# Optimization experiments

Measured on AMD Instinct MI355X. Metric: run time of the kernel, lower is better.

## Reference

```python
import jax, jax.numpy as jnp
import numpy as np

EPS = 1e-5
GROUPS = 32


def conv2d(x, w, b):
    # x: [N,C,H,W], w: [O,I,3,3] (or 1x1), stride 1, padding 'same' for 3x3
    kh = w.shape[2]
    pad = (kh - 1) // 2
    y = jax.lax.conv_general_dilated(x, w, (1, 1), ((pad, pad), (pad, pad)),
                                     dimension_numbers=('NCHW', 'OIHW', 'NCHW'))
    return y + b[None, :, None, None]


def group_norm(x, g, b):
    N, C, H, W = x.shape
    xr = x.reshape(N, GROUPS, C // GROUPS, H, W)
    mu = xr.mean(axis=(2, 3, 4), keepdims=True)
    var = xr.var(axis=(2, 3, 4), keepdims=True)
    xr = (xr - mu) / jnp.sqrt(var + EPS)
    return xr.reshape(N, C, H, W) * g[None, :, None, None] + b[None, :, None, None]


def batch_norm(x, g, b):
    # training-mode BatchNorm2d: batch statistics over (N,H,W)
    mu = x.mean(axis=(0, 2, 3), keepdims=True)
    var = x.var(axis=(0, 2, 3), keepdims=True)
    return (x - mu) / jnp.sqrt(var + EPS) * g[None, :, None, None] + b[None, :, None, None]


def binary_activation(x):
    # STE: forward sign(x), backward through piecewise poly out3
    out_fwd = jnp.sign(x)
    m1 = (x < -1).astype(x.dtype)
    m2 = (x < 0).astype(x.dtype)
    m3 = (x < 1).astype(x.dtype)
    out1 = -1.0 * m1 + (x * x + 2.0 * x) * (1.0 - m1)
    out2 = out1 * m2 + (-x * x + 2.0 * x) * (1.0 - m2)
    out3 = out2 * m3 + 1.0 * (1.0 - m3)
    return jax.lax.stop_gradient(out_fwd - out3) + out3


def hard_binary_conv(x, w, b):
    # per-output-channel scaling * sign(w), STE through clipped weights
    scale = jax.lax.stop_gradient(jnp.mean(jnp.abs(w), axis=(1, 2, 3), keepdims=True))
    bw_ng = scale * jnp.sign(w)
    clipped = jnp.clip(w, -1.0, 1.0)
    bw = jax.lax.stop_gradient(bw_ng - clipped) + clipped
    return conv2d(x, bw, b)


def learnable_bias(x, emb, w, b):
    bias = jax.nn.silu(emb) @ w.T + b  # [B, C]
    return x + bias[:, :, None, None]


def _forward(c, x, emb,
             rb_gn1_g, rb_gn1_b, rb_conv1_w, rb_conv1_b, rb_emb_w, rb_emb_b,
             rb_gn2_g, rb_gn2_b, rb_conv2_w, rb_conv2_b,
             m1_w, m1_b, bconv_w, bconv_b, bn_g, bn_b,
             m2_w, m2_b, prelu_a, m3_w, m3_b):
    # ResBlock (skip = Identity since out_channels == channels)
    h = conv2d(jax.nn.silu(group_norm(c, rb_gn1_g, rb_gn1_b)), rb_conv1_w, rb_conv1_b)
    eo = jax.nn.silu(emb) @ rb_emb_w.T + rb_emb_b          # [B, 2*C]
    scale, shift = jnp.split(eo[:, :, None, None], 2, axis=1)
    h = group_norm(h, rb_gn2_g, rb_gn2_b) * (1.0 + scale) + shift
    h = conv2d(jax.nn.silu(h), rb_conv2_w, rb_conv2_b)
    c2 = c + h
    # concat + bias + STE binarize + binary conv + BN + channel-pool residual + PReLU
    xc = jnp.concatenate([x, c2], axis=1)                   # [B, 2C, H, W]
    out = learnable_bias(xc, emb, m1_w, m1_b)
    out = binary_activation(out)
    out = hard_binary_conv(out, bconv_w, bconv_b)
    out = batch_norm(out, bn_g, bn_b)
    N, C2, H, W = xc.shape
    out = out + xc.reshape(N, C2 // 2, 2, H, W).mean(axis=2)  # channel mean pooling
    out = learnable_bias(out, emb, m2_w, m2_b)
    out = jnp.where(out >= 0, out, prelu_a[None, :, None, None] * out)  # PReLU
    out = learnable_bias(out, emb, m3_w, m3_b)
    return out


def setup_inputs() -> dict:
    key = jax.random.key(0)
    ks = jax.random.split(key, 24)
    B, C, EMB, H, W = 8, 128, 512, 64, 64
    IN2 = 2 * C
    n = lambda k, s, sc=0.05: jax.random.normal(k, s, dtype=jnp.float32) * sc
    return {
        'c': jax.random.normal(ks[0], (B, C, H, W), dtype=jnp.float32),
        'x': jax.random.normal(ks[1], (B, C, H, W), dtype=jnp.float32),
        'emb': jax.random.normal(ks[2], (B, EMB), dtype=jnp.float32),
        'rb_gn1_g': jnp.ones((C,), jnp.float32), 'rb_gn1_b': jnp.zeros((C,), jnp.float32),
        'rb_conv1_w': n(ks[3], (C, C, 3, 3)), 'rb_conv1_b': n(ks[4], (C,)),
        'rb_emb_w': n(ks[5], (2 * C, EMB)), 'rb_emb_b': n(ks[6], (2 * C,)),
        'rb_gn2_g': jnp.ones((C,), jnp.float32), 'rb_gn2_b': jnp.zeros((C,), jnp.float32),
        'rb_conv2_w': n(ks[7], (C, C, 3, 3)), 'rb_conv2_b': n(ks[8], (C,)),
        'm1_w': n(ks[9], (IN2, EMB)), 'm1_b': n(ks[10], (IN2,)),
        'bconv_w': jax.random.uniform(ks[11], (C, IN2, 3, 3), dtype=jnp.float32) * 0.001,
        'bconv_b': n(ks[12], (C,)),
        'bn_g': jnp.ones((C,), jnp.float32), 'bn_b': jnp.zeros((C,), jnp.float32),
        'm2_w': n(ks[13], (C, EMB)), 'm2_b': n(ks[14], (C,)),
        'prelu_a': jnp.full((C,), 0.25, jnp.float32),
        'm3_w': n(ks[15], (C, EMB)), 'm3_b': n(ks[16], (C,)),
    }


def reference(c, x, emb,
              rb_gn1_g, rb_gn1_b, rb_conv1_w, rb_conv1_b, rb_emb_w, rb_emb_b,
              rb_gn2_g, rb_gn2_b, rb_conv2_w, rb_conv2_b,
              m1_w, m1_b, bconv_w, bconv_b, bn_g, bn_b,
              m2_w, m2_b, prelu_a, m3_w, m3_b):
    return _forward(c, x, emb,
                    rb_gn1_g, rb_gn1_b, rb_conv1_w, rb_conv1_b, rb_emb_w, rb_emb_b,
                    rb_gn2_g, rb_gn2_b, rb_conv2_w, rb_conv2_b,
                    m1_w, m1_b, bconv_w, bconv_b, bn_g, bn_b,
                    m2_w, m2_b, prelu_a, m3_w, m3_b)
```

## Files before the change

kernel.cpp:

```cpp
#include <hip/hip_runtime.h>
#include <stdint.h>


#define B_   8
#define C_   128
#define C2_  256
#define HW_  4096
#define EMB_ 512
#define EPS_ 1e-5f

typedef int   v16i __attribute__((ext_vector_type(16)));
typedef float v16f __attribute__((ext_vector_type(16)));
typedef short v8s  __attribute__((ext_vector_type(8)));
typedef int   v4i  __attribute__((ext_vector_type(4)));

#define COLB 272
#define LDSZ (3 * 66 * COLB)
#define TSTRIDE 132

__device__ __forceinline__ float silu(float v) {
    return v * __builtin_amdgcn_rcpf(1.f + __expf(-v));
}
__device__ __forceinline__ unsigned short f2bf(float f) {
    unsigned int x = __float_as_uint(f);
    return (unsigned short)((x + 0x7FFFu + ((x >> 16) & 1u)) >> 16);
}
__device__ __forceinline__ int8_t sgn8(float v) {
    return (v > 0.f) ? (int8_t)1 : ((v < 0.f) ? (int8_t)(-1) : (int8_t)0);
}

__global__ __launch_bounds__(256) void k_prep(
    const float* __restrict__ w, int8_t* __restrict__ sgn,
    float* __restrict__ alpha, float* __restrict__ bnS, float* __restrict__ bnQ,
    float* __restrict__ gnS, float* __restrict__ gnQ,
    const float* __restrict__ w1, const float* __restrict__ w2,
    unsigned short* __restrict__ Wc1, unsigned short* __restrict__ Wc2,
    const float* __restrict__ emb,
    const float* __restrict__ ew, const float* __restrict__ ebb,
    const float* __restrict__ m1w, const float* __restrict__ m1b,
    const float* __restrict__ m2w, const float* __restrict__ m2b,
    const float* __restrict__ m3w, const float* __restrict__ m3b,
    float* __restrict__ eo, float* __restrict__ b1,
    float* __restrict__ b2, float* __restrict__ b3,
    const float* __restrict__ gin,
    float* __restrict__ g1S, float* __restrict__ g1Q) {
    __shared__ float red[256];
    const int blk = blockIdx.x, tid = threadIdx.x;
    if (blk < 128) {
        const int o = blk;
        if (o == 0 && tid < 128) { bnS[tid] = 0.f; bnQ[tid] = 0.f; }
        if (o == 1) { gnS[tid] = 0.f; }
        if (o == 2) { gnQ[tid] = 0.f; }
        const float* wr = w + (size_t)o * (C2_ * 9);
        float s = 0.f;
        for (int i = tid; i < C2_ * 9; i += 256) s += fabsf(wr[i]);
        red[tid] = s;
        __syncthreads();
        for (int st = 128; st > 0; st >>= 1) {
            if (tid < st) red[tid] += red[tid + st];
            __syncthreads();
        }
        if (tid == 0) alpha[o] = red[0] / (float)(C2_ * 9);
        for (int kk = 0; kk < 9; ++kk) {
            float v = wr[tid * 9 + kk];
            sgn[((size_t)(kk * 16 + (tid >> 4)) * C_ + o) * 16 + (tid & 15)] = sgn8(v);
        }
    } else if (blk < 704) {
        int i = (blk - 128) * 256 + tid;
        int co = i / (C_ * 9);
        int rem = i - co * (C_ * 9);
        int ci = rem / 9, kk = rem - ci * 9;
        size_t d = ((size_t)(kk * 16 + (ci >> 3)) * C_ + co) * 8 + (ci & 7);
        Wc1[d] = f2bf(w1[i]);
        Wc2[d] = f2bf(w2[i]);
    } else if (blk < 896) {
        const int o = (blk - 704) * 4 + (tid >> 6);
        const int l = tid & 63;
        const float* wv;
        float bias;
        float* dst;
        int dstride;
        if (o < 256)      { wv = ew  + (size_t)o * EMB_;              bias = ebb[o];    dst = eo + o;  dstride = 256; }
        else if (o < 512) { int r = o - 256; wv = m1w + (size_t)r * EMB_; bias = m1b[r]; dst = b1 + r; dstride = 256; }
        else if (o < 640) { int r = o - 512; wv = m2w + (size_t)r * EMB_; bias = m2b[r]; dst = b2 + r; dstride = 128; }
        else              { int r = o - 640; wv = m3w + (size_t)r * EMB_; bias = m3b[r]; dst = b3 + r; dstride = 128; }
        const float4 wa = *(const float4*)(wv + 8 * l);
        const float4 wb = *(const float4*)(wv + 8 * l + 4);
#pragma unroll
        for (int b = 0; b < B_; ++b) {
            const float* s = emb + b * EMB_ + 8 * l;
            float4 sa = *(const float4*)(s);
            float4 sb = *(const float4*)(s + 4);
            float p = wa.x * silu(sa.x) + wa.y * silu(sa.y) + wa.z * silu(sa.z) + wa.w * silu(sa.w) +
                      wb.x * silu(sb.x) + wb.y * silu(sb.y) + wb.z * silu(sb.z) + wb.w * silu(sb.w);
#pragma unroll
            for (int off = 32; off > 0; off >>= 1) p += __shfl_down(p, off, 64);
            if (l == 0) dst[b * dstride] = bias + p;
        }
    } else {
        const int bb = blk - 896;
        const int n = bb >> 5, grp = bb & 31;
        const size_t base = ((size_t)(n * C_ + grp * 4)) << 12;
        float sum = 0.f, sq = 0.f;
        const float4* in4 = (const float4*)(gin + base);
        for (int i = tid; i < 4096; i += 256) {
            float4 v = in4[i];
            sum += v.x + v.y + v.z + v.w;
            sq += v.x * v.x + v.y * v.y + v.z * v.z + v.w * v.w;
        }
#pragma unroll
        for (int off = 32; off > 0; off >>= 1) {
            sum += __shfl_xor(sum, off, 64);
            sq  += __shfl_xor(sq, off, 64);
        }
        if ((tid & 63) == 0) { red[tid >> 6] = sum; red[8 + (tid >> 6)] = sq; }
        __syncthreads();
        if (tid == 0) {
            g1S[n * 32 + grp] = red[0] + red[1] + red[2] + red[3];
            g1Q[n * 32 + grp] = red[8] + red[9] + red[10] + red[11];
        }
    }
}

__global__ __launch_bounds__(512, 4) void k_conv1(
    const float* __restrict__ cin,
    const unsigned short* __restrict__ Wc,
    const float* __restrict__ bias,
    const float* __restrict__ g1w, const float* __restrict__ g1b,
    const float* __restrict__ g1S, const float* __restrict__ g1Q,
    float* __restrict__ outN,
    float* __restrict__ gnS, float* __restrict__ gnQ) {
    __shared__ __align__(16) char lds[LDSZ];
    __shared__ float chA[128], chB[128];
    const int y = blockIdx.x;
    const int n = blockIdx.y;
    const int tid = threadIdx.x;

    if (tid < 128) {
        const int ch = tid, grp = tid >> 2;
        const float mu = g1S[n * 32 + grp] * (1.f / 16384.f);
        const float var = g1Q[n * 32 + grp] * (1.f / 16384.f) - mu * mu;
        const float rstd = rsqrtf(var + EPS_);
        const float A = g1w[ch] * rstd;
        chA[ch] = A;
        chB[ch] = g1b[ch] - mu * A;
    }
    if (tid < 96) {
        int r = tid / 32, q = tid & 31;
        int c = (q >> 4) ? 65 : 0, o = q & 15;
        *(float4*)(lds + (r * 66 + c) * COLB + o * 16) = make_float4(0.f, 0.f, 0.f, 0.f);
    }
    __syncthreads();

#pragma unroll
    for (int u = 0; u < 12; ++u) {
        int unit = u * 512 + tid;
        int r = unit >> 11, rem = unit & 2047;
        int ch = rem >> 4, seg = rem & 15;
        int yy = y - 1 + r;
        char* dst = lds + (r * 66 + 1 + seg) * COLB + 2 * ch;
        if (yy >= 0 && yy < 64) {
            const float A = chA[ch], Bv = chB[ch];
            const float* src = cin + (((size_t)(n * C_ + ch)) << 12) + yy * 64 + seg;
#pragma unroll
            for (int j = 0; j < 4; ++j)
                *(unsigned short*)(dst + (16 * j) * COLB) = f2bf(silu(src[16 * j] * A + Bv));
        } else {
#pragma unroll
            for (int j = 0; j < 4; ++j)
                *(unsigned short*)(dst + (16 * j) * COLB) = 0;
        }
    }
    __syncthreads();

    const int w = tid >> 6;
    const int og = w >> 1;
    const int ph = w & 1;
    const int l = tid & 63;
    const int lm = l & 31;
    const int lh = l >> 5;

    v16f acc;
#pragma unroll
    for (int i = 0; i < 16; ++i) acc[i] = 0.f;

#pragma unroll
    for (int kk = 0; kk < 9; ++kk) {
        const int r = kk / 3, dx = kk % 3 - 1;
        const char* col = lds + (r * 66 + 32 * ph + lm + 1 + dx) * COLB + 16 * lh;
        const unsigned short* wbase = Wc + (size_t)(kk * 16 + lh) * C_ * 8 + (32 * og + lm) * 8;
#pragma unroll
        for (int cb = 0; cb < 8; ++cb) {
            v8s a = *(const v8s*)(wbase + (size_t)(2 * cb) * C_ * 8);
            v8s b = *(const v8s*)(col + 32 * cb);
            acc = __builtin_amdgcn_mfma_f32_32x32x16_bf16(a, b, acc, 0, 0, 0);
        }
    }
    __syncthreads();
    float* ldsT = (float*)lds;
    float* ldsS = (float*)(lds + 64 * TSTRIDE * 4);
    float* ldsQ = ldsS + 256;
#pragma unroll
    for (int r = 0; r < 16; ++r) {
        const int row = (r & 3) + 8 * (r >> 2) + 4 * lh;
        const int co = 32 * og + row;
        float v = acc[r] + bias[co];
        ldsT[(32 * ph + lm) * TSTRIDE + co] = v;
        float p = v, q = v * v;
#pragma unroll
        for (int m = 16; m > 0; m >>= 1) {
            p += __shfl_xor(p, m, 64);
            q += __shfl_xor(q, m, 64);
        }
        if (lm == 0) { ldsS[ph * 128 + co] = p; ldsQ[ph * 128 + co] = q; }
    }
    __syncthreads();
    if (tid < 32) {
        const int g = tid;
        float p = 0.f, q = 0.f;
#pragma unroll
        for (int j = 0; j < 4; ++j) {
            p += ldsS[4 * g + j] + ldsS[128 + 4 * g + j];
            q += ldsQ[4 * g + j] + ldsQ[128 + 4 * g + j];
        }
        atomicAdd(&gnS[n * 32 + g], p);
        atomicAdd(&gnQ[n * 32 + g], q);
    }
    const int q4 = tid & 31;
    float* orow = outN + (((size_t)(n * HW_) + (y << 6)) << 7);
#pragma unroll
    for (int it = 0; it < 4; ++it) {
        const int px = it * 16 + (tid >> 5);
        *(float4*)(orow + ((size_t)px << 7) + 4 * q4) =
            *(const float4*)(ldsT + px * TSTRIDE + 4 * q4);
    }
}

__global__ __launch_bounds__(512, 4) void k_conv2(
    const float* __restrict__ yin,
    const unsigned short* __restrict__ Wc,
    const float* __restrict__ bias,
    const float* __restrict__ res,
    const float* __restrict__ xin,
    const float* __restrict__ b1v,
    const float* __restrict__ eo,
    const float* __restrict__ g2,
    const float* __restrict__ bt2,
    const float* __restrict__ gnS,
    const float* __restrict__ gnQ,
    float* __restrict__ poolC2,
    int8_t* __restrict__ S) {
    __shared__ __align__(16) char lds[LDSZ];
    __shared__ float ldsA[128], ldsB[128];
    const int y = blockIdx.x;
    const int n = blockIdx.y;
    const int tid = threadIdx.x;

    if (tid < 128) {
        const int ch = tid, grp = tid >> 2;
        const float mu = gnS[n * 32 + grp] * (1.f / 16384.f);
        const float var = gnQ[n * 32 + grp] * (1.f / 16384.f) - mu * mu;
        const float rstd = rsqrtf(var + EPS_);
        const float gg = g2[ch] * rstd;
        const float sc = 1.f + eo[n * 256 + ch];
        ldsA[ch] = gg * sc;
        ldsB[ch] = (bt2[ch] - mu * gg) * sc + eo[n * 256 + 128 + ch];
    }
    if (tid < 96) {
        int r = tid / 32, q = tid & 31;
        int cpad = (q >> 4) ? 65 : 0, o = q & 15;
        *(float4*)(lds + (r * 66 + cpad) * COLB + o * 16) = make_float4(0.f, 0.f, 0.f, 0.f);
    }
    __syncthreads();

    const int qc = tid & 31;
    const float A0 = ldsA[4 * qc], A1 = ldsA[4 * qc + 1], A2 = ldsA[4 * qc + 2], A3 = ldsA[4 * qc + 3];
    const float B0 = ldsB[4 * qc], B1 = ldsB[4 * qc + 1], B2 = ldsB[4 * qc + 2], B3 = ldsB[4 * qc + 3];
#pragma unroll
    for (int r = 0; r < 3; ++r) {
        const int yy = y - 1 + r;
        const float* ysrc = yin + (((size_t)(n * HW_) + yy * 64) << 7);
        const bool ok = (yy >= 0 && yy < 64);
#pragma unroll
        for (int it = 0; it < 4; ++it) {
            const int px = it * 16 + (tid >> 5);
            char* dst = lds + (r * 66 + px + 1) * COLB + qc * 8;
            if (ok) {
                float4 v = *(const float4*)(ysrc + ((size_t)px << 7) + 4 * qc);
                union { unsigned short u[4]; uint2 q; } pk;
                pk.u[0] = f2bf(silu(v.x * A0 + B0));
                pk.u[1] = f2bf(silu(v.y * A1 + B1));
                pk.u[2] = f2bf(silu(v.z * A2 + B2));
                pk.u[3] = f2bf(silu(v.w * A3 + B3));
                *(uint2*)dst = pk.q;
            } else {
                *(uint2*)dst = make_uint2(0u, 0u);
            }
        }
    }
    __syncthreads();

    const int w = tid >> 6;
    const int og = w >> 1;
    const int ph = w & 1;
    const int l = tid & 63;
    const int lm = l & 31;
    const int lh = l >> 5;

    v16f acc;
#pragma unroll
    for (int i = 0; i < 16; ++i) acc[i] = 0.f;

#pragma unroll
    for (int kk = 0; kk < 9; ++kk) {
        const int r = kk / 3, dx = kk % 3 - 1;
        const char* col = lds + (r * 66 + 32 * ph + lm + 1 + dx) * COLB + 16 * lh;
        const unsigned short* wbase = Wc + (size_t)(kk * 16 + lh) * C_ * 8 + (32 * og + lm) * 8;
#pragma unroll
        for (int cb = 0; cb < 8; ++cb) {
            v8s a = *(const v8s*)(wbase + (size_t)(2 * cb) * C_ * 8);
            v8s b = *(const v8s*)(col + 32 * cb);
            acc = __builtin_amdgcn_mfma_f32_32x32x16_bf16(a, b, acc, 0, 0, 0);
        }
    }
    float c2v[16];
#pragma unroll
    for (int r = 0; r < 16; ++r) {
        const int row = (r & 3) + 8 * (r >> 2) + 4 * lh;
        const int co = 32 * og + row;
        const size_t o = (((size_t)n * C_ + co) << 12) + (y << 6);
        c2v[r] = acc[r] + bias[co] + res[o + 32 * ph + lm];
    }
#pragma unroll
    for (int q = 0; q < 4; ++q) {
        const int pc = 16 * og + 4 * q + 2 * lh;
        const size_t po = (((size_t)n * 64 + pc) << 12) + (y << 6);
        poolC2[po + 32 * ph + lm]        = 0.5f * (c2v[4 * q] + c2v[4 * q + 1]);
        poolC2[po + 4096 + 32 * ph + lm] = 0.5f * (c2v[4 * q + 2] + c2v[4 * q + 3]);
    }

    __syncthreads();
#pragma unroll
    for (int q = 0; q < 4; ++q) {
        const int co0 = 32 * og + 8 * q + 4 * lh;
        const float b0 = b1v[n * 256 + 128 + co0];
        const float b1b = b1v[n * 256 + 128 + co0 + 1];
        const float b2b = b1v[n * 256 + 128 + co0 + 2];
        const float b3b = b1v[n * 256 + 128 + co0 + 3];
        union { int8_t b[4]; int u; } p0;
        p0.b[0] = sgn8(c2v[4 * q] + b0);
        p0.b[1] = sgn8(c2v[4 * q + 1] + b1b);
        p0.b[2] = sgn8(c2v[4 * q + 2] + b2b);
        p0.b[3] = sgn8(c2v[4 * q + 3] + b3b);
        *(int*)(lds + (32 * ph + lm) * COLB + 128 + co0) = p0.u;
    }
#pragma unroll
    for (int u = 0; u < 4; ++u) {
        int idx = u * 512 + tid;
        int ch = idx >> 4, seg = idx & 15;
        float4 v = *(const float4*)(xin + (((size_t)(n * C_ + ch)) << 12) + (y << 6) + 4 * seg);
        const float bv = b1v[n * 256 + ch];
        lds[(4 * seg) * COLB + ch]     = sgn8(v.x + bv);
        lds[(4 * seg + 1) * COLB + ch] = sgn8(v.y + bv);
        lds[(4 * seg + 2) * COLB + ch] = sgn8(v.z + bv);
        lds[(4 * seg + 3) * COLB + ch] = sgn8(v.w + bv);
    }
    __syncthreads();
    int8_t* Srow = S + ((size_t)(n * HW_) + (y << 6)) * C2_;
#pragma unroll
    for (int u = 0; u < 2; ++u) {
        int idx = u * 512 + tid;
        int px = idx >> 4, c16 = idx & 15;
        *(int4*)(Srow + (size_t)px * C2_ + 16 * c16) = *(const int4*)(lds + px * COLB + 16 * c16);
    }
}

__global__ __launch_bounds__(512, 4) void k_bconv(
    const int8_t* __restrict__ S,
    const int8_t* __restrict__ Wk,
    const float* __restrict__ alpha,
    const float* __restrict__ bias,
    float* __restrict__ out,
    float* __restrict__ bnS, float* __restrict__ bnQ) {
    __shared__ __align__(16) char lds[LDSZ];
    const int y = blockIdx.x;
    const int n = blockIdx.y;
    const int tid = threadIdx.x;
    const char* base = (const char*)(S + ((size_t)n * 64) * 64 * C2_);
    const char* r0 = (y > 0)  ? base + (size_t)(y - 1) * 16384 : nullptr;
    const char* r1 = base + (size_t)y * 16384;
    const char* r2 = (y < 63) ? base + (size_t)(y + 1) * 16384 : nullptr;
    if (tid < 96) {
        int r = tid / 32, q = tid & 31;
        int c = (q >> 4) ? 65 : 0, o = q & 15;
        *(float4*)(lds + (r * 66 + c) * COLB + o * 16) = make_float4(0.f, 0.f, 0.f, 0.f);
    }
    {
        const char* rs0 = r0; const char* rs1 = r1; const char* rs2 = r2;
#pragma unroll
        for (int it = 0; it < 2; ++it) {
            int idx = it * 512 + tid;
            int x = idx >> 4, o = idx & 15;
            char* d0 = lds + (0 * 66 + x + 1) * COLB + o * 16;
            char* d1 = lds + (1 * 66 + x + 1) * COLB + o * 16;
            char* d2 = lds + (2 * 66 + x + 1) * COLB + o * 16;
            if (rs0) *(float4*)d0 = *(const float4*)(rs0 + x * 256 + o * 16);
            else     *(float4*)d0 = make_float4(0.f, 0.f, 0.f, 0.f);
            *(float4*)d1 = *(const float4*)(rs1 + x * 256 + o * 16);
            if (rs2) *(float4*)d2 = *(const float4*)(rs2 + x * 256 + o * 16);
            else     *(float4*)d2 = make_float4(0.f, 0.f, 0.f, 0.f);
        }
    }
    __syncthreads();

    const int w = tid >> 6;
    const int og = w >> 1;
    const int ph = w & 1;
    const int l = tid & 63;
    const int lm = l & 31;
    const int lh = l >> 5;

    v16i acc;
#pragma unroll
    for (int i = 0; i < 16; ++i) acc[i] = 0;

#pragma unroll
    for (int kk = 0; kk < 9; ++kk) {
        const int r = kk / 3, dx = kk % 3 - 1;
        const char* col = lds + (r * 66 + 32 * ph + lm + 1 + dx) * COLB + 16 * lh;
        const int8_t* wbase = Wk + (size_t)(kk * 16 + lh) * C_ * 16 + (32 * og + lm) * 16;
#pragma unroll
        for (int s = 0; s < 8; ++s) {
            v4i a = *(const v4i*)(wbase + (size_t)(2 * s) * C_ * 16);
            v4i b = *(const v4i*)(col + 32 * s);
            acc = __builtin_amdgcn_mfma_i32_32x32x32_i8(a, b, acc, 0, 0, 0);
        }
    }
    __syncthreads();
    float* ldsS = (float*)lds;
    float* ldsQ = (float*)lds + 256;
#pragma unroll
    for (int r = 0; r < 16; ++r) {
        const int row = (r & 3) + 8 * (r >> 2) + 4 * lh;
        const int co = 32 * og + row;
        const float av = alpha[co], bv = bias[co];
        const size_t o = (((size_t)n * C_ + co) << 12) + (y << 6);
        float v = av * (float)acc[r] + bv;
        out[o + 32 * ph + lm] = v;
        float p = v, q = v * v;
#pragma unroll
        for (int m = 16; m > 0; m >>= 1) {
            p += __shfl_xor(p, m, 64);
            q += __shfl_xor(q, m, 64);
        }
        if (lm == 0) { ldsS[ph * 128 + co] = p; ldsQ[ph * 128 + co] = q; }
    }
    __syncthreads();
    if (tid < 128) {
        atomicAdd(&bnS[tid], ldsS[tid] + ldsS[128 + tid]);
        atomicAdd(&bnQ[tid], ldsQ[tid] + ldsQ[128 + tid]);
    }
}

__global__ __launch_bounds__(256) void k_final(const float* __restrict__ y3,
                                               const float* __restrict__ x,
                                               const float* __restrict__ poolC2,
                                               const float* __restrict__ bnS,
                                               const float* __restrict__ bnQ,
                                               const float* __restrict__ bng,
                                               const float* __restrict__ bnb,
                                               const float* __restrict__ b2v,
                                               const float* __restrict__ pa,
                                               const float* __restrict__ b3v,
                                               float* __restrict__ out) {
    const int idx4 = blockIdx.x * 256 + threadIdx.x;
    const int hw = (idx4 & 1023) * 4;
    const int cb = idx4 >> 10;
    const int co = cb & 127;
    const int n = cb >> 7;
    const float mu = bnS[co] * (1.f / 32768.f);
    const float var = bnQ[co] * (1.f / 32768.f) - mu * mu;
    const float rstd = rsqrtf(var + EPS_);
    const float gm = rstd * bng[co];
    const float bt = bnb[co] - mu * gm;
    const size_t obase = (((size_t)(n * C_ + co)) << 12) + hw;
    float4 v = *(const float4*)(y3 + obase);
    v.x = v.x * gm + bt; v.y = v.y * gm + bt; v.z = v.z * gm + bt; v.w = v.w * gm + bt;

    float4 pv;
    if (co < 64) {
        const int ch0 = 2 * co;
        float4 pA = *(const float4*)(x + (((size_t)(n * C_ + ch0)) << 12) + hw);
        float4 pB = *(const float4*)(x + (((size_t)(n * C_ + ch0 + 1)) << 12) + hw);
        pv.x = 0.5f * (pA.x + pB.x); pv.y = 0.5f * (pA.y + pB.y);
        pv.z = 0.5f * (pA.z + pB.z); pv.w = 0.5f * (pA.w + pB.w);
    } else {
        pv = *(const float4*)(poolC2 + (((size_t)(n * 64 + co - 64)) << 12) + hw);
    }
    const float bias2 = b2v[n * 128 + co];
    const float aP = pa[co];
    const float bias3 = b3v[n * 128 + co];
    float4 r;
    float t;
    t = v.x + pv.x + bias2; t = (t >= 0.f) ? t : aP * t; r.x = t + bias3;
    t = v.y + pv.y + bias2; t = (t >= 0.f) ? t : aP * t; r.y = t + bias3;
    t = v.z + pv.z + bias2; t = (t >= 0.f) ? t : aP * t; r.z = t + bias3;
    t = v.w + pv.w + bias2; t = (t >= 0.f) ? t : aP * t; r.w = t + bias3;
    *(float4*)(out + obase) = r;
}

extern "C" void kernel_launch(void* const* d_in, const int* in_sizes, int n_in,
                              void* d_out, int out_size, void* d_ws, size_t ws_size,
                              hipStream_t stream) {
    const float* c       = (const float*)d_in[0];
    const float* x       = (const float*)d_in[1];
    const float* emb     = (const float*)d_in[2];
    const float* gn1_g   = (const float*)d_in[3];
    const float* gn1_b   = (const float*)d_in[4];
    const float* conv1_w = (const float*)d_in[5];
    const float* conv1_b = (const float*)d_in[6];
    const float* emb_w   = (const float*)d_in[7];
    const float* emb_b   = (const float*)d_in[8];
    const float* gn2_g   = (const float*)d_in[9];
    const float* gn2_b   = (const float*)d_in[10];
    const float* conv2_w = (const float*)d_in[11];
    const float* conv2_b = (const float*)d_in[12];
    const float* m1_w    = (const float*)d_in[13];
    const float* m1_b    = (const float*)d_in[14];
    const float* bconv_w = (const float*)d_in[15];
    const float* bconv_b = (const float*)d_in[16];
    const float* bn_g    = (const float*)d_in[17];
    const float* bn_b    = (const float*)d_in[18];
    const float* m2_w    = (const float*)d_in[19];
    const float* m2_b    = (const float*)d_in[20];
    const float* prelu_a = (const float*)d_in[21];
    const float* m3_w    = (const float*)d_in[22];
    const float* m3_b    = (const float*)d_in[23];
    float* out = (float*)d_out;

    float* ws = (float*)d_ws;
    const size_t NCHW = (size_t)B_ * C_ * HW_;
    float*  poolC2 = ws;
    float*  y_buf = ws + NCHW;
    int8_t* S     = (int8_t*)(ws + 2 * NCHW);
    int8_t* sgn   = (int8_t*)(ws + 2 * NCHW + NCHW / 2);
    unsigned short* Wc1 = (unsigned short*)(ws + 2 * NCHW + NCHW / 2 + 73728);
    unsigned short* Wc2 = Wc1 + C_ * C_ * 9;
    float*  alpha = ws + 2 * NCHW + NCHW / 2 + 73728 + 2 * 73728;
    float*  eo    = alpha + 128;
    float*  b1v   = eo + B_ * 256;
    float*  b2v   = b1v + B_ * 256;
    float*  b3v   = b2v + B_ * 128;
    float*  bnS   = b3v + B_ * 128;
    float*  bnQ   = bnS + 128;
    float*  gnS   = bnQ + 128;
    float*  gnQ   = gnS + 256;
    float*  g1S   = gnQ + 256;
    float*  g1Q   = g1S + 256;

    k_prep<<<1152, 256, 0, stream>>>(bconv_w, sgn, alpha, bnS, bnQ, gnS, gnQ,
                                     conv1_w, conv2_w, Wc1, Wc2,
                                     emb, emb_w, emb_b, m1_w, m1_b, m2_w, m2_b,
                                     m3_w, m3_b, eo, b1v, b2v, b3v,
                                     c, g1S, g1Q);
    k_conv1<<<dim3(64, B_), 512, 0, stream>>>(c, Wc1, conv1_b, gn1_g, gn1_b,
                                              g1S, g1Q, y_buf, gnS, gnQ);
    k_conv2<<<dim3(64, B_), 512, 0, stream>>>(y_buf, Wc2, conv2_b, c, x, b1v, eo,
                                              gn2_g, gn2_b, gnS, gnQ, poolC2, S);
    k_bconv<<<dim3(64, B_), 512, 0, stream>>>(S, sgn, alpha, bconv_b, y_buf, bnS, bnQ);
    k_final<<<NCHW / 1024, 256, 0, stream>>>(y_buf, x, poolC2, bnS, bnQ, bn_g, bn_b,
                                             b2v, prelu_a, b3v, out);
}
```

Before: 219.3 us.

## Store padded sign tensor in LDS layout and stream it with direct global-to-LDS loads

After: 216.3 us. Within noise of the previous version (-1.4%).

```diff
diff --git a/kernel.cpp b/kernel.cpp
--- a/kernel.cpp
+++ b/kernel.cpp
@@ -15,7 +15,8 @@
 typedef int   v4i  __attribute__((ext_vector_type(4)));
 
 #define COLB 272
-#define LDSZ (3 * 66 * COLB)
+#define ROWB (66 * COLB)
+#define LDSZ 55296
 #define TSTRIDE 132
 
 __device__ __forceinline__ float silu(float v) {
@@ -27,6 +28,10 @@
 }
 __device__ __forceinline__ int8_t sgn8(float v) {
     return (v > 0.f) ? (int8_t)1 : ((v < 0.f) ? (int8_t)(-1) : (int8_t)0);
+}
+__device__ __forceinline__ void gld16(char* ldst, const char* gsrc) {
+    __builtin_amdgcn_global_load_lds((const unsigned int*)gsrc,
+                                     (unsigned int*)ldst, 16, 0, 0);
 }
 
 __global__ __launch_bounds__(256) void k_prep(
@@ -43,7 +48,8 @@
     float* __restrict__ eo, float* __restrict__ b1,
     float* __restrict__ b2, float* __restrict__ b3,
     const float* __restrict__ gin,
-    float* __restrict__ g1S, float* __restrict__ g1Q) {
+    float* __restrict__ g1S, float* __restrict__ g1Q,
+    int8_t* __restrict__ S) {
     __shared__ float red[256];
     const int blk = blockIdx.x, tid = threadIdx.x;
     if (blk < 128) {
@@ -97,13 +103,13 @@
             for (int off = 32; off > 0; off >>= 1) p += __shfl_down(p, off, 64);
             if (l == 0) dst[b * dstride] = bias + p;
         }
-    } else {
-        const int bb = blk - 896;
-        const int n = bb >> 5, grp = bb & 31;
+    } else if (blk < 1408) {
+        const int idx = blk - 896;
+        const int n = idx >> 6, rest = idx & 63, grp = rest >> 1, h = rest & 1;
         const size_t base = ((size_t)(n * C_ + grp * 4)) << 12;
         float sum = 0.f, sq = 0.f;
         const float4* in4 = (const float4*)(gin + base);
-        for (int i = tid; i < 4096; i += 256) {
+        for (int i = tid + h * 2048; i < (h + 1) * 2048; i += 256) {
             float4 v = in4[i];
             sum += v.x + v.y + v.z + v.w;
             sq += v.x * v.x + v.y * v.y + v.z * v.z + v.w * v.w;
@@ -116,9 +122,16 @@
         if ((tid & 63) == 0) { red[tid >> 6] = sum; red[8 + (tid >> 6)] = sq; }
         __syncthreads();
         if (tid == 0) {
-            g1S[n * 32 + grp] = red[0] + red[1] + red[2] + red[3];
-            g1Q[n * 32 + grp] = red[8] + red[9] + red[10] + red[11];
-        }
+            g1S[h * 256 + n * 32 + grp] = red[0] + red[1] + red[2] + red[3];
+            g1Q[h * 256 + n * 32 + grp] = red[8] + red[9] + red[10] + red[11];
+        }
+    } else {
+        const int u = blk - 1408;
+        const int n = u >> 1;
+        const int row = (u & 1) * 65;
+        int4* base = (int4*)(S + (size_t)n * 66 * ROWB + (size_t)row * ROWB);
+        const int4 z = make_int4(0, 0, 0, 0);
+        for (int i = tid; i < ROWB / 16; i += 256) base[i] = z;
     }
 }
 
@@ -138,8 +151,10 @@
 
     if (tid < 128) {
         const int ch = tid, grp = tid >> 2;
-        const float mu = g1S[n * 32 + grp] * (1.f / 16384.f);
-        const float var = g1Q[n * 32 + grp] * (1.f / 16384.f) - mu * mu;
+        const float s1 = g1S[n * 32 + grp] + g1S[256 + n * 32 + grp];
+        const float q1 = g1Q[n * 32 + grp] + g1Q[256 + n * 32 + grp];
+        const float mu = s1 * (1.f / 16384.f);
+        const float var = q1 * (1.f / 16384.f) - mu * mu;
         const float rstd = rsqrtf(var + EPS_);
         const float A = g1w[ch] * rstd;
         chA[ch] = A;
@@ -152,23 +167,32 @@
     }
     __syncthreads();
 
-#pragma unroll
-    for (int u = 0; u < 12; ++u) {
+    union F4 { float4 v; float f[4]; };
+#pragma unroll
+    for (int u = 0; u < 6; ++u) {
         int unit = u * 512 + tid;
-        int r = unit >> 11, rem = unit & 2047;
-        int ch = rem >> 4, seg = rem & 15;
+        int r = unit >> 10, rem = unit & 1023;
+        int cp = rem >> 4, s4 = rem & 15;
+        int ch0 = 2 * cp;
         int yy = y - 1 + r;
-        char* dst = lds + (r * 66 + 1 + seg) * COLB + 2 * ch;
+        char* dst0 = lds + (r * 66 + 4 * s4 + 1) * COLB + 4 * cp;
         if (yy >= 0 && yy < 64) {
-            const float A = chA[ch], Bv = chB[ch];
-            const float* src = cin + (((size_t)(n * C_ + ch)) << 12) + yy * 64 + seg;
-#pragma unroll
-            for (int j = 0; j < 4; ++j)
-                *(unsigned short*)(dst + (16 * j) * COLB) = f2bf(silu(src[16 * j] * A + Bv));
+            const float* src = cin + (((size_t)(n * C_ + ch0)) << 12) + yy * 64 + 4 * s4;
+            F4 fa, fb;
+            fa.v = *(const float4*)src;
+            fb.v = *(const float4*)(src + HW_);
+            const float A0 = chA[ch0], B0 = chB[ch0];
+            const float A1 = chA[ch0 + 1], B1 = chB[ch0 + 1];
+#pragma unroll
+            for (int e = 0; e < 4; ++e) {
+                unsigned int lo = f2bf(silu(fa.f[e] * A0 + B0));
+                unsigned int hi = f2bf(silu(fb.f[e] * A1 + B1));
+                *(unsigned int*)(dst0 + e * COLB) = lo | (hi << 16);
+            }
         } else {
 #pragma unroll
-            for (int j = 0; j < 4; ++j)
-                *(unsigned short*)(dst + (16 * j) * COLB) = 0;
+            for (int e = 0; e < 4; ++e)
+                *(unsigned int*)(dst0 + e * COLB) = 0u;
         }
     }
     __syncthreads();
@@ -352,7 +376,7 @@
         p0.b[1] = sgn8(c2v[4 * q + 1] + b1b);
         p0.b[2] = sgn8(c2v[4 * q + 2] + b2b);
         p0.b[3] = sgn8(c2v[4 * q + 3] + b3b);
-        *(int*)(lds + (32 * ph + lm) * COLB + 128 + co0) = p0.u;
+        *(int*)(lds + (32 * ph + lm + 1) * COLB + 128 + co0) = p0.u;
     }
 #pragma unroll
     for (int u = 0; u < 4; ++u) {
@@ -360,19 +384,19 @@
         int ch = idx >> 4, seg = idx & 15;
         float4 v = *(const float4*)(xin + (((size_t)(n * C_ + ch)) << 12) + (y << 6) + 4 * seg);
         const float bv = b1v[n * 256 + ch];
-        lds[(4 * seg) * COLB + ch]     = sgn8(v.x + bv);
-        lds[(4 * seg + 1) * COLB + ch] = sgn8(v.y + bv);
-        lds[(4 * seg + 2) * COLB + ch] = sgn8(v.z + bv);
-        lds[(4 * seg + 3) * COLB + ch] = sgn8(v.w + bv);
-    }
-    __syncthreads();
-    int8_t* Srow = S + ((size_t)(n * HW_) + (y << 6)) * C2_;
-#pragma unroll
-    for (int u = 0; u < 2; ++u) {
-        int idx = u * 512 + tid;
-        int px = idx >> 4, c16 = idx & 15;
-        *(int4*)(Srow + (size_t)px * C2_ + 16 * c16) = *(const int4*)(lds + px * COLB + 16 * c16);
-    }
+        lds[(4 * seg + 1) * COLB + ch]     = sgn8(v.x + bv);
+        lds[(4 * seg + 2) * COLB + ch] = sgn8(v.y + bv);
+        lds[(4 * seg + 3) * COLB + ch] = sgn8(v.z + bv);
+        lds[(4 * seg + 4) * COLB + ch] = sgn8(v.w + bv);
+    }
+    if (tid < 34) {
+        int c = tid / 17, o = tid - c * 17;
+        *(float4*)(lds + (c ? 65 : 0) * COLB + o * 16) = make_float4(0.f, 0.f, 0.f, 0.f);
+    }
+    __syncthreads();
+    int4* Srow = (int4*)(S + (size_t)n * 66 * ROWB + (size_t)(y + 1) * ROWB);
+    const int4* lsrc = (const int4*)lds;
+    for (int i = tid; i < ROWB / 16; i += 512) Srow[i] = lsrc[i];
 }
 
 __global__ __launch_bounds__(512, 4) void k_bconv(
@@ -386,31 +410,10 @@
     const int y = blockIdx.x;
     const int n = blockIdx.y;
     const int tid = threadIdx.x;
-    const char* base = (const char*)(S + ((size_t)n * 64) * 64 * C2_);
-    const char* r0 = (y > 0)  ? base + (size_t)(y - 1) * 16384 : nullptr;
-    const char* r1 = base + (size_t)y * 16384;
-    const char* r2 = (y < 63) ? base + (size_t)(y + 1) * 16384 : nullptr;
-    if (tid < 96) {
-        int r = tid / 32, q = tid & 31;
-        int c = (q >> 4) ? 65 : 0, o = q & 15;
-        *(float4*)(lds + (r * 66 + c) * COLB + o * 16) = make_float4(0.f, 0.f, 0.f, 0.f);
-    }
-    {
-        const char* rs0 = r0; const char* rs1 = r1; const char* rs2 = r2;
-#pragma unroll
-        for (int it = 0; it < 2; ++it) {
-            int idx = it * 512 + tid;
-            int x = idx >> 4, o = idx & 15;
-            char* d0 = lds + (0 * 66 + x + 1) * COLB + o * 16;
-            char* d1 = lds + (1 * 66 + x + 1) * COLB + o * 16;
-            char* d2 = lds + (2 * 66 + x + 1) * COLB + o * 16;
-            if (rs0) *(float4*)d0 = *(const float4*)(rs0 + x * 256 + o * 16);
-            else     *(float4*)d0 = make_float4(0.f, 0.f, 0.f, 0.f);
-            *(float4*)d1 = *(const float4*)(rs1 + x * 256 + o * 16);
-            if (rs2) *(float4*)d2 = *(const float4*)(rs2 + x * 256 + o * 16);
-            else     *(float4*)d2 = make_float4(0.f, 0.f, 0.f, 0.f);
-        }
-    }
+    const char* src3 = (const char*)S + (size_t)n * 66 * ROWB + (size_t)y * ROWB;
+    const int wave = tid >> 6, lane = tid & 63;
+    for (int u = wave; u < 53; u += 8)
+        gld16(lds + u * 1024, src3 + u * 1024 + lane * 16);
     __syncthreads();
 
     const int w = tid >> 6;
@@ -543,10 +546,11 @@
     float*  poolC2 = ws;
     float*  y_buf = ws + NCHW;
     int8_t* S     = (int8_t*)(ws + 2 * NCHW);
-    int8_t* sgn   = (int8_t*)(ws + 2 * NCHW + NCHW / 2);
-    unsigned short* Wc1 = (unsigned short*)(ws + 2 * NCHW + NCHW / 2 + 73728);
+    const size_t S_f = (8 * 66 * (size_t)ROWB) / 4 + 256;
+    int8_t* sgn   = (int8_t*)(ws + 2 * NCHW + S_f);
+    unsigned short* Wc1 = (unsigned short*)(ws + 2 * NCHW + S_f + 73728);
     unsigned short* Wc2 = Wc1 + C_ * C_ * 9;
-    float*  alpha = ws + 2 * NCHW + NCHW / 2 + 73728 + 2 * 73728;
+    float*  alpha = ws + 2 * NCHW + S_f + 73728 + 2 * 73728;
     float*  eo    = alpha + 128;
     float*  b1v   = eo + B_ * 256;
     float*  b2v   = b1v + B_ * 256;
@@ -556,13 +560,13 @@
     float*  gnS   = bnQ + 128;
     float*  gnQ   = gnS + 256;
     float*  g1S   = gnQ + 256;
-    float*  g1Q   = g1S + 256;
-
-    k_prep<<<1152, 256, 0, stream>>>(bconv_w, sgn, alpha, bnS, bnQ, gnS, gnQ,
+    float*  g1Q   = g1S + 512;
+
+    k_prep<<<1424, 256, 0, stream>>>(bconv_w, sgn, alpha, bnS, bnQ, gnS, gnQ,
                                      conv1_w, conv2_w, Wc1, Wc2,
                                      emb, emb_w, emb_b, m1_w, m1_b, m2_w, m2_b,
                                      m3_w, m3_b, eo, b1v, b2v, b3v,
-                                     c, g1S, g1Q);
+                                     c, g1S, g1Q, S);
     k_conv1<<<dim3(64, B_), 512, 0, stream>>>(c, Wc1, conv1_b, gn1_g, gn1_b,
                                               g1S, g1Q, y_buf, gnS, gnQ);
     k_conv2<<<dim3(64, B_), 512, 0, stream>>>(y_buf, Wc2, conv2_b, c, x, b1v, eo,
```
